# Kernel optimization log

Measured on AMD Instinct MI355X. Metric: run time of the kernel, lower is better.

The kernel has to match this reference:

```python
import jax, jax.numpy as jnp
import numpy as np

D = 512            # model size
H = 8              # num_heads
HD = D // H        # head_size = 64
WIN = 7            # num_keys (payload tokens per window)
QNB = 5            # query_nb for 'mean' aggregation
SCALE = D ** -0.5  # NOTE: torch module scales by size**-0.5, not head_size**-0.5
EPS = 1e-5


def setup_inputs() -> dict:
    key = jax.random.key(0)
    ks = jax.random.split(key, 12)
    B, M = 8, 4096
    w = lambda i: jax.random.normal(ks[i], (D, D), jnp.float32) * 0.02
    return {
        "k": jax.random.normal(ks[0], (B, M, D), jnp.float32),
        "v": jax.random.normal(ks[1], (B, M, D), jnp.float32),
        "q": jax.random.normal(ks[2], (B, M, D), jnp.float32),
        "query_len": 3584,
        "Wk": w(3), "bk": jnp.zeros((D,), jnp.float32),
        "Wv": w(4), "bv": jnp.zeros((D,), jnp.float32),
        "Wq": w(5), "bq": jnp.zeros((D,), jnp.float32),
        "ln_g": jnp.ones((D,), jnp.float32), "ln_b": jnp.zeros((D,), jnp.float32),
        "Wpq": w(6), "bpq": jnp.zeros((D,), jnp.float32),
        "Wpk": w(7), "bpk": jnp.zeros((D,), jnp.float32),
        "Wo": w(8), "bo": jnp.zeros((D,), jnp.float32),
    }


def reference(k, v, q, query_len, Wk, bk, Wv, bv, Wq, bq, ln_g, ln_b, Wpq, bpq, Wpk, bpk, Wo, bo):
    B, M, _ = k.shape
    win_num = -(-query_len // WIN)     # ceil
    per_win = M // win_num

    k = k @ Wk + bk
    v = v @ Wv + bv
    q = q @ Wq + bq

    # 'mean' query aggregation: AvgPool1d(kernel=QNB, stride=1, pad=QNB//2),
    # count_include_pad=True => always divide by QNB (zero-padded)
    qp = jnp.pad(q, ((0, 0), (QNB // 2, QNB // 2), (0, 0)))
    q = sum(qp[:, j:j + M] for j in range(QNB)) / QNB

    # ---- stage 1: DSA (local attention inside each window of per_win tokens)
    resh = lambda x: x.reshape(B, win_num, per_win, H, HD).transpose(0, 1, 3, 2, 4)
    dq, dk, dv = resh(q), resh(k), resh(v)                       # [B,W,H,p,hd]
    attn = jax.nn.softmax(jnp.einsum('bwhqd,bwhkd->bwhqk', dq, dk) * SCALE, axis=-1)
    out = jnp.einsum('bwhqk,bwhkd->bwhqd', attn, dv)
    out = out.transpose(0, 1, 3, 2, 4).reshape(B, win_num, per_win, D)

    win_tok = out[:, :, 0, :]          # [B, W, D] window summary tokens
    attn_x = out[:, :, 1:, :]

    # LayerNorm + exact GELU on window tokens
    mu = win_tok.mean(-1, keepdims=True)
    var = ((win_tok - mu) ** 2).mean(-1, keepdims=True)
    win_tok = (win_tok - mu) / jnp.sqrt(var + EPS) * ln_g + ln_b
    win_tok = jax.nn.gelu(win_tok, approximate=False)

    # ---- stage 2: PSA (attention over window summary tokens)
    pq = (win_tok @ Wpq + bpq).reshape(B, win_num, H, HD).transpose(0, 2, 1, 3)  # [B,H,W,hd]
    pk = (win_tok @ Wpk + bpk).reshape(B, win_num, H, HD).transpose(0, 2, 1, 3)
    pv = attn_x.reshape(B, win_num, WIN, H, HD).transpose(0, 3, 1, 2, 4)
    pv = pv.reshape(B, H, win_num, WIN * HD)

    pattn = jax.nn.softmax(jnp.einsum('bhqd,bhkd->bhqk', pq, pk) * SCALE, axis=-1)
    pout = jnp.einsum('bhqk,bhkd->bhqd', pattn, pv)
    pout = pout.transpose(0, 2, 1, 3).reshape(B, win_num, H, WIN, HD)
    pout = pout.transpose(0, 1, 3, 2, 4).reshape(B, win_num, WIN, D)

    out = (pout + attn_x).reshape(B, win_num * WIN, D)[:, :query_len, :]
    return out @ Wo + bo
```

## Files before the change

kernel.cpp:

```cpp
#include <hip/hip_runtime.h>
#include <hip/hip_bf16.h>
#include <math.h>

#define SCALE_ 0.04419417382415922f
#define EPS_  1e-5f

typedef unsigned short u16;
typedef __attribute__((ext_vector_type(8))) short     bf16x8;
typedef __attribute__((ext_vector_type(4))) float     f32x4;
typedef __attribute__((ext_vector_type(8))) unsigned short u16x8;
typedef __attribute__((ext_vector_type(4))) unsigned short u16x4;

__device__ __forceinline__ u16 f2b(float f) {
  union { float f; unsigned int u; } x; x.f = f;
  unsigned int u = x.u;
  return (u16)((u + 0x7FFFu + ((u >> 16) & 1u)) >> 16);
}
__device__ __forceinline__ float b2f(u16 h) {
  union { unsigned int u; float f; } x; x.u = ((unsigned int)h) << 16;
  return x.f;
}
__device__ __forceinline__ void gload_lds16(const void* g, void* l) {
  __builtin_amdgcn_global_load_lds(
      (const __attribute__((address_space(1))) void*)g,
      (__attribute__((address_space(3))) void*)l, 16, 0, 0);
}

__global__ __launch_bounds__(256) void wconv(
    const float* W0, const float* W1, const float* W2,
    const float* W3, const float* W4, const float* W5, u16* wt)
{
  const float* W;
  switch (blockIdx.z) {
    case 0: W = W0; break; case 1: W = W1; break; case 2: W = W2; break;
    case 3: W = W3; break; case 4: W = W4; break; default: W = W5; break;
  }
  u16* Wt = wt + (size_t)blockIdx.z * 262144;
  const int k0 = blockIdx.x * 64, n0 = blockIdx.y * 64;
  __shared__ float T[64][68];
  const int tid = threadIdx.x;
#pragma unroll
  for (int it = 0; it < 4; ++it) {
    int L = it * 256 + tid;
    int r = L >> 4, cg = L & 15;
    float4 v = *reinterpret_cast<const float4*>(W + (size_t)(k0 + r) * 512 + n0 + cg * 4);
    T[r][cg * 4 + 0] = v.x; T[r][cg * 4 + 1] = v.y;
    T[r][cg * 4 + 2] = v.z; T[r][cg * 4 + 3] = v.w;
  }
  __syncthreads();
#pragma unroll
  for (int it = 0; it < 2; ++it) {
    int L = it * 256 + tid;
    int rn = L >> 3, kg = L & 7;
    u16x8 o;
#pragma unroll
    for (int e = 0; e < 8; ++e) o[e] = f2b(T[kg * 8 + e][rn]);
    *(u16x8*)(Wt + (size_t)(n0 + rn) * 512 + k0 + kg * 8) = o;
  }
}

__global__ __launch_bounds__(512) void gemm_proj(
    const float* A0, const u16* Bt0, const float* bi0, u16* C0,
    const float* A1, const u16* Bt1, const float* bi1, u16* C1,
    const float* A2, const u16* Bt2, const float* bi2, u16* C2)
{
  const float *A, *bias; const u16* Bt; u16* C;
  if (blockIdx.z == 0)      { A = A0; Bt = Bt0; bias = bi0; C = C0; }
  else if (blockIdx.z == 1) { A = A1; Bt = Bt1; bias = bi1; C = C1; }
  else                      { A = A2; Bt = Bt2; bias = bi2; C = C2; }

  __shared__ u16 As[2][4096];
  __shared__ u16 Bs[2][16384];
  const int tid = threadIdx.x;
  const int lane = tid & 63, wid = tid >> 6;
  const int wr = wid >> 2, wcn = wid & 3;
  const int l15 = lane & 15, lh = lane >> 4;
  const int sx = (l15 >> 1) & 3;
  const int m0 = blockIdx.x * 128;

  const int rr = tid >> 2, sp = tid & 3;
  const int ssw = sp ^ ((rr >> 1) & 3);

  const f32x4 fz = {0.f, 0.f, 0.f, 0.f};
  f32x4 acc[4][8];
#pragma unroll
  for (int m = 0; m < 4; ++m)
#pragma unroll
    for (int n = 0; n < 8; ++n) acc[m][n] = fz;

  const int aoff0 = (wr * 64 + l15) * 64 + ((lh ^ sx) << 4);
  const int boff0 = (wcn * 128 + l15) * 64 + ((lh ^ sx) << 4);

  {
#pragma unroll
    for (int it = 0; it < 4; ++it)
      gload_lds16(Bt + (size_t)(it * 128 + rr) * 512 + ssw * 8,
                  (char*)Bs[0] + (it * 512 + wid * 64) * 16);
    const float* ga = A + (size_t)(m0 + rr) * 512 + ssw * 8;
    float4 x0 = *reinterpret_cast<const float4*>(ga);
    float4 x1 = *reinterpret_cast<const float4*>(ga + 4);
    u16x8 o;
    o[0] = f2b(x0.x); o[1] = f2b(x0.y); o[2] = f2b(x0.z); o[3] = f2b(x0.w);
    o[4] = f2b(x1.x); o[5] = f2b(x1.y); o[6] = f2b(x1.z); o[7] = f2b(x1.w);
    *(u16x8*)((char*)As[0] + tid * 16) = o;
  }
  __syncthreads();

#pragma unroll 2
  for (int t = 0; t < 16; ++t) {
    const int cur = t & 1, nxt = cur ^ 1;
    float4 x0 = {0.f,0.f,0.f,0.f}, x1 = {0.f,0.f,0.f,0.f};
    if (t < 15) {
      const int k0 = (t + 1) * 32;
#pragma unroll
      for (int it = 0; it < 4; ++it)
        gload_lds16(Bt + (size_t)(it * 128 + rr) * 512 + k0 + ssw * 8,
                    (char*)Bs[nxt] + (it * 512 + wid * 64) * 16);
      const float* ga = A + (size_t)(m0 + rr) * 512 + k0 + ssw * 8;
      x0 = *reinterpret_cast<const float4*>(ga);
      x1 = *reinterpret_cast<const float4*>(ga + 4);
    }
    bf16x8 af[4], bfr[8];
#pragma unroll
    for (int m = 0; m < 4; ++m)
      af[m] = *(const bf16x8*)((const char*)As[cur] + aoff0 + m * 1024);
#pragma unroll
    for (int n = 0; n < 8; ++n)
      bfr[n] = *(const bf16x8*)((const char*)Bs[cur] + boff0 + n * 1024);
#pragma unroll
    for (int m = 0; m < 4; ++m)
#pragma unroll
      for (int n = 0; n < 8; ++n)
        acc[m][n] = __builtin_amdgcn_mfma_f32_16x16x32_bf16(af[m], bfr[n], acc[m][n], 0, 0, 0);
    if (t < 15) {
      u16x8 o;
      o[0] = f2b(x0.x); o[1] = f2b(x0.y); o[2] = f2b(x0.z); o[3] = f2b(x0.w);
      o[4] = f2b(x1.x); o[5] = f2b(x1.y); o[6] = f2b(x1.z); o[7] = f2b(x1.w);
      *(u16x8*)((char*)As[nxt] + tid * 16) = o;
    }
    __syncthreads();
  }

  const int gn0 = wcn * 128 + l15;
  float bv[8];
#pragma unroll
  for (int n = 0; n < 8; ++n) bv[n] = bias[gn0 + n * 16];
#pragma unroll
  for (int m = 0; m < 4; ++m)
#pragma unroll
    for (int reg = 0; reg < 4; ++reg) {
      int gm = m0 + wr * 64 + m * 16 + lh * 4 + reg;
#pragma unroll
      for (int n = 0; n < 8; ++n)
        C[(size_t)gm * 512 + gn0 + n * 16] = f2b(acc[m][n][reg] + bv[n]);
    }
}

__global__ __launch_bounds__(512) void gemm_out(
    const u16* __restrict__ A, const u16* __restrict__ Bt,
    const float* __restrict__ bias, float* __restrict__ C)
{
  __shared__ u16 As[2][4096];
  __shared__ u16 Bs[2][16384];
  const int tid = threadIdx.x;
  const int lane = tid & 63, wid = tid >> 6;
  const int wr = wid >> 2, wcn = wid & 3;
  const int l15 = lane & 15, lh = lane >> 4;
  const int sx = (l15 >> 1) & 3;
  const int m0 = blockIdx.x * 128;
  const int rr = tid >> 2, sp = tid & 3;
  const int ssw = sp ^ ((rr >> 1) & 3);

  const f32x4 fz = {0.f, 0.f, 0.f, 0.f};
  f32x4 acc[4][8];
#pragma unroll
  for (int m = 0; m < 4; ++m)
#pragma unroll
    for (int n = 0; n < 8; ++n) acc[m][n] = fz;

  const int aoff0 = (wr * 64 + l15) * 64 + ((lh ^ sx) << 4);
  const int boff0 = (wcn * 128 + l15) * 64 + ((lh ^ sx) << 4);

  {
#pragma unroll
    for (int it = 0; it < 4; ++it)
      gload_lds16(Bt + (size_t)(it * 128 + rr) * 512 + ssw * 8,
                  (char*)Bs[0] + (it * 512 + wid * 64) * 16);
    gload_lds16(A + (size_t)(m0 + rr) * 512 + ssw * 8,
                (char*)As[0] + (wid * 64) * 16);
  }
  __syncthreads();

#pragma unroll 2
  for (int t = 0; t < 16; ++t) {
    const int cur = t & 1, nxt = cur ^ 1;
    if (t < 15) {
      const int k0 = (t + 1) * 32;
#pragma unroll
      for (int it = 0; it < 4; ++it)
        gload_lds16(Bt + (size_t)(it * 128 + rr) * 512 + k0 + ssw * 8,
                    (char*)Bs[nxt] + (it * 512 + wid * 64) * 16);
      gload_lds16(A + (size_t)(m0 + rr) * 512 + k0 + ssw * 8,
                  (char*)As[nxt] + (wid * 64) * 16);
    }
    bf16x8 af[4], bfr[8];
#pragma unroll
    for (int m = 0; m < 4; ++m)
      af[m] = *(const bf16x8*)((const char*)As[cur] + aoff0 + m * 1024);
#pragma unroll
    for (int n = 0; n < 8; ++n)
      bfr[n] = *(const bf16x8*)((const char*)Bs[cur] + boff0 + n * 1024);
#pragma unroll
    for (int m = 0; m < 4; ++m)
#pragma unroll
      for (int n = 0; n < 8; ++n)
        acc[m][n] = __builtin_amdgcn_mfma_f32_16x16x32_bf16(af[m], bfr[n], acc[m][n], 0, 0, 0);
    __syncthreads();
  }

  const int gn0 = wcn * 128 + l15;
  float bv[8];
#pragma unroll
  for (int n = 0; n < 8; ++n) bv[n] = bias[gn0 + n * 16];
#pragma unroll
  for (int m = 0; m < 4; ++m)
#pragma unroll
    for (int reg = 0; reg < 4; ++reg) {
      int gm = m0 + wr * 64 + m * 16 + lh * 4 + reg;
#pragma unroll
      for (int n = 0; n < 8; ++n)
        C[(size_t)gm * 512 + gn0 + n * 16] = acc[m][n][reg] + bv[n];
    }
}

__global__ __launch_bounds__(256) void gemm_pp(
    const u16* __restrict__ A,
    const u16* __restrict__ Bt0, const float* __restrict__ bi0, u16* __restrict__ C0,
    const u16* __restrict__ Bt1, const float* __restrict__ bi1, u16* __restrict__ C1)
{
  const u16* Bt; const float* bias; u16* C;
  if (blockIdx.z == 0) { Bt = Bt0; bias = bi0; C = C0; }
  else                 { Bt = Bt1; bias = bi1; C = C1; }

  __shared__ u16 As[8192];
  __shared__ u16 Bs[8192];
  const int tid = threadIdx.x;
  const int lane = tid & 63, wid = tid >> 6;
  const int wr = wid >> 1, wc = wid & 1;
  const int l15 = lane & 15, lh = lane >> 4, l7 = lane & 7;
  const int m0 = blockIdx.x * 128, n0 = blockIdx.y * 128;

  const f32x4 fz = {0.f, 0.f, 0.f, 0.f};
  f32x4 acc[4][4];
#pragma unroll
  for (int m = 0; m < 4; ++m)
#pragma unroll
    for (int n = 0; n < 4; ++n) acc[m][n] = fz;

  int aoff[2], boff[2];
#pragma unroll
  for (int kh = 0; kh < 2; ++kh) {
    int slot = ((kh * 4 + lh) ^ l7) << 4;
    aoff[kh] = (wr * 64 + l15) * 128 + slot;
    boff[kh] = (wc * 64 + l15) * 128 + slot;
  }

  for (int k0 = 0; k0 < 512; k0 += 64) {
    __syncthreads();
#pragma unroll
    for (int it = 0; it < 4; ++it) {
      int L = it * 256 + tid;
      int r = L >> 3, s = L & 7;
      int c = s ^ (r & 7);
      gload_lds16(A  + (size_t)(m0 + r) * 512 + k0 + c * 8,
                  (char*)As + (it * 256 + wid * 64) * 16);
      gload_lds16(Bt + (size_t)(n0 + r) * 512 + k0 + c * 8,
                  (char*)Bs + (it * 256 + wid * 64) * 16);
    }
    __syncthreads();
#pragma unroll
    for (int kh = 0; kh < 2; ++kh) {
      bf16x8 af[4], bfr[4];
#pragma unroll
      for (int m = 0; m < 4; ++m)
        af[m] = *(const bf16x8*)((const char*)As + aoff[kh] + m * 2048);
#pragma unroll
      for (int n = 0; n < 4; ++n)
        bfr[n] = *(const bf16x8*)((const char*)Bs + boff[kh] + n * 2048);
#pragma unroll
      for (int m = 0; m < 4; ++m)
#pragma unroll
        for (int n = 0; n < 4; ++n)
          acc[m][n] = __builtin_amdgcn_mfma_f32_16x16x32_bf16(af[m], bfr[n], acc[m][n], 0, 0, 0);
    }
  }

  const int gn0 = n0 + wc * 64 + l15;
  float bv[4];
#pragma unroll
  for (int n = 0; n < 4; ++n) bv[n] = bias[gn0 + n * 16];
#pragma unroll
  for (int m = 0; m < 4; ++m)
#pragma unroll
    for (int reg = 0; reg < 4; ++reg) {
      int gm = m0 + wr * 64 + m * 16 + lh * 4 + reg;
#pragma unroll
      for (int n = 0; n < 4; ++n)
        C[(size_t)gm * 512 + gn0 + n * 16] = f2b(acc[m][n][reg] + bv[n]);
    }
}

__global__ __launch_bounds__(256) void qk_mfma(
    const u16* __restrict__ pq, const u16* __restrict__ pk, u16* __restrict__ expS)
{
  __shared__ u16 As[8192];
  __shared__ u16 Bs[8192];
  const int tid = threadIdx.x;
  const int lane = tid & 63, wid = tid >> 6;
  const int wr = wid >> 1, wc = wid & 1;
  const int l15 = lane & 15, lh = lane >> 4, l7 = lane & 7;
  const int bh = blockIdx.z, b = bh >> 3, h = bh & 7;
  const int wq0 = blockIdx.x * 128, wk0 = blockIdx.y * 128;

  const f32x4 fz = {0.f, 0.f, 0.f, 0.f};
  f32x4 acc[4][4];
#pragma unroll
  for (int m = 0; m < 4; ++m)
#pragma unroll
    for (int n = 0; n < 4; ++n) acc[m][n] = fz;

#pragma unroll
  for (int it = 0; it < 4; ++it) {
    int L = it * 256 + tid;
    int r = L >> 3, s = L & 7;
    int c = s ^ (r & 7);
    gload_lds16(pq + ((size_t)b * 512 + wq0 + r) * 512 + h * 64 + c * 8,
                (char*)As + (it * 256 + wid * 64) * 16);
    gload_lds16(pk + ((size_t)b * 512 + wk0 + r) * 512 + h * 64 + c * 8,
                (char*)Bs + (it * 256 + wid * 64) * 16);
  }
  __syncthreads();

#pragma unroll
  for (int kh = 0; kh < 2; ++kh) {
    int slot = ((kh * 4 + lh) ^ l7) << 4;
    int aoff = (wr * 64 + l15) * 128 + slot;
    int boff = (wc * 64 + l15) * 128 + slot;
    bf16x8 af[4], bfr[4];
#pragma unroll
    for (int m = 0; m < 4; ++m)
      af[m] = *(const bf16x8*)((const char*)As + aoff + m * 2048);
#pragma unroll
    for (int n = 0; n < 4; ++n)
      bfr[n] = *(const bf16x8*)((const char*)Bs + boff + n * 2048);
#pragma unroll
    for (int m = 0; m < 4; ++m)
#pragma unroll
      for (int n = 0; n < 4; ++n)
        acc[m][n] = __builtin_amdgcn_mfma_f32_16x16x32_bf16(af[m], bfr[n], acc[m][n], 0, 0, 0);
  }

  const int gn0 = wk0 + wc * 64 + l15;
#pragma unroll
  for (int m = 0; m < 4; ++m)
#pragma unroll
    for (int reg = 0; reg < 4; ++reg) {
      int gm = wq0 + wr * 64 + m * 16 + lh * 4 + reg;
#pragma unroll
      for (int n = 0; n < 4; ++n)
        expS[((size_t)bh * 512 + gm) * 512 + gn0 + n * 16] =
            f2b(expf(acc[m][n][reg] * SCALE_));
    }
}

__global__ __launch_bounds__(64) void attn_win(
    const u16* kp, const u16* vp, const u16* qp0, u16* attn)
{
  const int h = blockIdx.x, w = blockIdx.y, b = blockIdx.z;
  const int t = threadIdx.x;
  __shared__ float ks[8][68], vs[8][68], qr[12][68], qs[8][68], Ps[8][9];
  const size_t base = ((size_t)b * 4096 + (size_t)w * 8) * 512 + h * 64;

  {
    int i = t >> 3, dg = t & 7;
    u16x8 kv = *(const u16x8*)(kp + base + (size_t)i * 512 + dg * 8);
    u16x8 vv = *(const u16x8*)(vp + base + (size_t)i * 512 + dg * 8);
#pragma unroll
    for (int e = 0; e < 8; ++e) {
      ks[i][dg * 8 + e] = b2f(kv[e]);
      vs[i][dg * 8 + e] = b2f(vv[e]);
    }
  }
#pragma unroll
  for (int l = 0; l < 2; ++l) {
    int L = t + l * 64;
    if (L < 96) {
      int i = L >> 3, dg = L & 7;
      int m = w * 8 - 2 + i;
      if (m >= 0 && m < 4096) {
        u16x8 qv = *(const u16x8*)(qp0 + ((size_t)b * 4096 + m) * 512 + h * 64 + dg * 8);
#pragma unroll
        for (int e = 0; e < 8; ++e) qr[i][dg * 8 + e] = b2f(qv[e]);
      } else {
#pragma unroll
        for (int e = 0; e < 8; ++e) qr[i][dg * 8 + e] = 0.0f;
      }
    }
  }
  __syncthreads();
#pragma unroll
  for (int j = 0; j < 8; ++j)
    qs[j][t] = 0.2f * (qr[j][t] + qr[j + 1][t] + qr[j + 2][t] + qr[j + 3][t] + qr[j + 4][t]);
  __syncthreads();

  const int qi = t >> 3, kj = t & 7;
  float s = 0.0f;
#pragma unroll
  for (int d = 0; d < 64; ++d) s = fmaf(qs[qi][d], ks[kj][d], s);
  s *= SCALE_;
  float mx = s;
  mx = fmaxf(mx, __shfl_xor(mx, 1));
  mx = fmaxf(mx, __shfl_xor(mx, 2));
  mx = fmaxf(mx, __shfl_xor(mx, 4));
  float e = expf(s - mx);
  float sum = e;
  sum += __shfl_xor(sum, 1);
  sum += __shfl_xor(sum, 2);
  sum += __shfl_xor(sum, 4);
  Ps[qi][kj] = e / sum;
  __syncthreads();

  float o[8];
#pragma unroll
  for (int c = 0; c < 8; ++c) o[c] = 0.0f;
#pragma unroll
  for (int tt = 0; tt < 8; ++tt) {
    float pw = Ps[qi][tt];
#pragma unroll
    for (int c = 0; c < 8; ++c) o[c] = fmaf(pw, vs[tt][kj * 8 + c], o[c]);
  }
  u16x8 ov;
#pragma unroll
  for (int c = 0; c < 8; ++c) ov[c] = f2b(o[c]);
  *(u16x8*)(attn + base + (size_t)qi * 512 + kj * 8) = ov;
}

__global__ __launch_bounds__(256) void pvt_build(const u16* attn, u16* pvT)
{
  const int bh = blockIdx.x;
  const int b = bh >> 3, h = bh & 7;
  const int w0 = blockIdx.y * 32;
  __shared__ u16 TL[448 * 40];
  const int tid = threadIdx.x;
#pragma unroll
  for (int it = 0; it < 8; ++it) {
    int L = it * 256 + tid;
    int dg = L & 7, r = L >> 3;
    int w2l = r >> 3, tt = r & 7;
    if (tt < 7) {
      int m = 8 * (w0 + w2l) + tt + 1;
      u16x8 v = *(const u16x8*)(attn + ((size_t)b * 4096 + m) * 512 + h * 64 + dg * 8);
#pragma unroll
      for (int e = 0; e < 8; ++e)
        TL[(tt * 64 + dg * 8 + e) * 40 + w2l] = v[e];
    }
  }
  __syncthreads();
#pragma unroll
  for (int it = 0; it < 7; ++it) {
    int L = it * 256 + tid;
    int n = L >> 2, seg = L & 3;
    u16x8 v = *(const u16x8*)(&TL[n * 40 + seg * 8]);
    *(u16x8*)(pvT + ((size_t)bh * 448 + n) * 512 + w0 + seg * 8) = v;
  }
}

__global__ __launch_bounds__(64) void ln_gelu(
    const u16* attn, const float* g, const float* be, u16* wt)
{
  const int r = blockIdx.x;
  const int b = r >> 9, w = r & 511;
  const int t = threadIdx.x;
  const u16* x = attn + (((size_t)b * 4096) + (size_t)w * 8) * 512;

  u16x8 v = *(const u16x8*)(x + t * 8);
  float xv[8];
  float s1 = 0.f, s2 = 0.f;
#pragma unroll
  for (int e = 0; e < 8; ++e) {
    xv[e] = b2f(v[e]);
    s1 += xv[e]; s2 += xv[e] * xv[e];
  }
#pragma unroll
  for (int off = 1; off < 64; off <<= 1) {
    s1 += __shfl_xor(s1, off);
    s2 += __shfl_xor(s2, off);
  }
  const float mu  = s1 * (1.0f / 512.0f);
  const float var = s2 * (1.0f / 512.0f) - mu * mu;
  const float inv = 1.0f / sqrtf(var + EPS_);

  const int d0 = t * 8;
  float4 g0 = *reinterpret_cast<const float4*>(g + d0);
  float4 g1 = *reinterpret_cast<const float4*>(g + d0 + 4);
  float4 b0 = *reinterpret_cast<const float4*>(be + d0);
  float4 b1 = *reinterpret_cast<const float4*>(be + d0 + 4);
  float gv[8] = {g0.x, g0.y, g0.z, g0.w, g1.x, g1.y, g1.z, g1.w};
  float bvv[8] = {b0.x, b0.y, b0.z, b0.w, b1.x, b1.y, b1.z, b1.w};
  const float k2 = 0.70710678118654752f;
  u16x8 ov;
#pragma unroll
  for (int e = 0; e < 8; ++e) {
    float y = (xv[e] - mu) * inv * gv[e] + bvv[e];
    ov[e] = f2b(0.5f * y * (1.0f + erff(y * k2)));
  }
  *(u16x8*)(wt + (size_t)r * 512 + d0) = ov;
}

__global__ __launch_bounds__(256) void rs_inv(const u16* expS, float* rsinv)
{
  const int row = blockIdx.x * 4 + (threadIdx.x >> 6);
  const int t = threadIdx.x & 63;
  u16x8 v = *(const u16x8*)(expS + (size_t)row * 512 + t * 8);
  float s = 0.f;
#pragma unroll
  for (int e = 0; e < 8; ++e) s += b2f(v[e]);
#pragma unroll
  for (int off = 1; off < 64; off <<= 1) s += __shfl_xor(s, off);
  if (t == 0) rsinv[row] = 1.0f / s;
}

__global__ __launch_bounds__(256) void pv_mfma(
    const u16* __restrict__ expS, const u16* __restrict__ pvT,
    const float* __restrict__ rsinv, const u16* __restrict__ attn,
    u16* __restrict__ X2)
{
  __shared__ u16 As[8192];
  __shared__ u16 Bs[4096];
  const int tid = threadIdx.x;
  const int lane = tid & 63, wid = tid >> 6;
  const int wr = wid >> 1, wc = wid & 1;
  const int l15 = lane & 15, lh = lane >> 4, l7 = lane & 7;
  const int bh = blockIdx.z, b = bh >> 3, h = bh & 7;
  const int m0 = blockIdx.x * 128;
  const int nt = blockIdx.y;

  const f32x4 fz = {0.f, 0.f, 0.f, 0.f};
  f32x4 acc[4][2];
#pragma unroll
  for (int m = 0; m < 4; ++m)
#pragma unroll
    for (int n = 0; n < 2; ++n) acc[m][n] = fz;

  int aoff[2], boff[2];
#pragma unroll
  for (int kh = 0; kh < 2; ++kh) {
    int slot = ((kh * 4 + lh) ^ l7) << 4;
    aoff[kh] = (wr * 64 + l15) * 128 + slot;
    boff[kh] = (wc * 32 + l15) * 128 + slot;
  }

  for (int k0 = 0; k0 < 512; k0 += 64) {
    __syncthreads();
#pragma unroll
    for (int it = 0; it < 4; ++it) {
      int L = it * 256 + tid;
      int r = L >> 3, s = L & 7;
      int c = s ^ (r & 7);
      gload_lds16(expS + ((size_t)bh * 512 + m0 + r) * 512 + k0 + c * 8,
                  (char*)As + (it * 256 + wid * 64) * 16);
    }
#pragma unroll
    for (int it = 0; it < 2; ++it) {
      int L = it * 256 + tid;
      int r = L >> 3, s = L & 7;
      int c = s ^ (r & 7);
      gload_lds16(pvT + ((size_t)bh * 448 + nt * 64 + r) * 512 + k0 + c * 8,
                  (char*)Bs + (it * 256 + wid * 64) * 16);
    }
    __syncthreads();
#pragma unroll
    for (int kh = 0; kh < 2; ++kh) {
      bf16x8 af[4], bfr[2];
#pragma unroll
      for (int m = 0; m < 4; ++m)
        af[m] = *(const bf16x8*)((const char*)As + aoff[kh] + m * 2048);
#pragma unroll
      for (int n = 0; n < 2; ++n)
        bfr[n] = *(const bf16x8*)((const char*)Bs + boff[kh] + n * 2048);
#pragma unroll
      for (int m = 0; m < 4; ++m)
#pragma unroll
        for (int n = 0; n < 2; ++n)
          acc[m][n] = __builtin_amdgcn_mfma_f32_16x16x32_bf16(af[m], bfr[n], acc[m][n], 0, 0, 0);
    }
  }

#pragma unroll
  for (int m = 0; m < 4; ++m)
#pragma unroll
    for (int reg = 0; reg < 4; ++reg) {
      int gm = m0 + wr * 64 + m * 16 + lh * 4 + reg;
      float ri = rsinv[bh * 512 + gm];
#pragma unroll
      for (int n = 0; n < 2; ++n) {
        int d = wc * 32 + n * 16 + l15;
        float res = b2f(attn[((size_t)b * 4096 + gm * 8 + nt + 1) * 512 + h * 64 + d]);
        X2[((size_t)b * 3584 + gm * 7 + nt) * 512 + h * 64 + d] =
            f2b(acc[m][n][reg] * ri + res);
      }
    }
}

extern "C" void kernel_launch(void* const* d_in, const int* in_sizes, int n_in,
                              void* d_out, int out_size, void* d_ws, size_t ws_size,
                              hipStream_t stream)
{
  const float* k_in = (const float*)d_in[0];
  const float* v_in = (const float*)d_in[1];
  const float* q_in = (const float*)d_in[2];
  const float* Wk  = (const float*)d_in[4];
  const float* bk  = (const float*)d_in[5];
  const float* Wv  = (const float*)d_in[6];
  const float* bv  = (const float*)d_in[7];
  const float* Wq  = (const float*)d_in[8];
  const float* bq  = (const float*)d_in[9];
  const float* lng = (const float*)d_in[10];
  const float* lnb = (const float*)d_in[11];
  const float* Wpq = (const float*)d_in[12];
  const float* bpq = (const float*)d_in[13];
  const float* Wpk = (const float*)d_in[14];
  const float* bpk = (const float*)d_in[15];
  const float* Wo  = (const float*)d_in[16];
  const float* bo  = (const float*)d_in[17];
  float* out = (float*)d_out;

  char* ws = (char*)d_ws;
  const size_t MB = 1024 * 1024;
  u16* wtb  = (u16*)(ws);
  u16* kp   = (u16*)(ws + 16 * MB);
  u16* vp   = (u16*)(ws + 52 * MB);
  u16* qp0  = (u16*)(ws + 88 * MB);
  u16* attn = (u16*)(ws + 124 * MB);
  u16*   wt    = (u16*)(ws + 16 * MB);
  u16*   pq    = (u16*)(ws + 20 * MB);
  u16*   pk    = (u16*)(ws + 28 * MB);
  float* rsinv = (float*)(ws + 36 * MB);
  u16*   expS  = (u16*)(ws + 40 * MB);
  u16*   pvT   = (u16*)(ws + 76 * MB);
  u16*   X2    = (u16*)(ws + 160 * MB);

  u16* Wkt  = wtb;
  u16* Wvt  = wtb + 1 * 262144;
  u16* Wqt  = wtb + 2 * 262144;
  u16* Wpqt = wtb + 3 * 262144;
  u16* Wpkt = wtb + 4 * 262144;
  u16* Wot  = wtb + 5 * 262144;

  wconv<<<dim3(8, 8, 6), 256, 0, stream>>>(Wk, Wv, Wq, Wpq, Wpk, Wo, wtb);

  gemm_proj<<<dim3(256, 1, 3), 512, 0, stream>>>(
      k_in, Wkt, bk, kp,
      v_in, Wvt, bv, vp,
      q_in, Wqt, bq, qp0);

  attn_win<<<dim3(8, 512, 8), 64, 0, stream>>>(kp, vp, qp0, attn);
  pvt_build<<<dim3(64, 16), 256, 0, stream>>>(attn, pvT);
  ln_gelu<<<4096, 64, 0, stream>>>(attn, lng, lnb, wt);

  gemm_pp<<<dim3(32, 4, 2), 256, 0, stream>>>(
      wt, Wpqt, bpq, pq, Wpkt, bpk, pk);

  qk_mfma<<<dim3(4, 4, 64), 256, 0, stream>>>(pq, pk, expS);
  rs_inv<<<8192, 256, 0, stream>>>(expS, rsinv);
  pv_mfma<<<dim3(4, 7, 64), 256, 0, stream>>>(expS, pvT, rsinv, attn, X2);

  gemm_out<<<dim3(224, 1, 1), 512, 0, stream>>>(X2, Wot, bo, out);
}
```

Baseline: 281.1 us.

## Retile projection GEMM to 128x128 blocks with direct global B fragment loads

The QKV projection GEMM changes from a 512-thread block covering 128 rows by the full 512 columns to a 256-thread block covering 128x128 tiles, launched over four column tiles. B fragments are now read straight from global memory into registers rather than staged in LDS, and the A tile uses a 64-wide k-step with XOR swizzling. This cuts LDS use and raises occupancy, at the cost of reading and converting the fp32 A rows four times and issuing uncached-in-LDS B loads. Separately, the pv_mfma grid swaps its x and y dimensions so neighbouring blocks share the same row tile.

```diff
diff --git a/kernel.cpp b/kernel.cpp
--- a/kernel.cpp
+++ b/kernel.cpp
@@ -59,7 +59,7 @@
   }
 }
 
-__global__ __launch_bounds__(512) void gemm_proj(
+__global__ __launch_bounds__(256, 3) void gemm_proj(
     const float* A0, const u16* Bt0, const float* bi0, u16* C0,
     const float* A1, const u16* Bt1, const float* bi1, u16* C1,
     const float* A2, const u16* Bt2, const float* bi2, u16* C2)
@@ -69,89 +69,110 @@
   else if (blockIdx.z == 1) { A = A1; Bt = Bt1; bias = bi1; C = C1; }
   else                      { A = A2; Bt = Bt2; bias = bi2; C = C2; }
 
-  __shared__ u16 As[2][4096];
-  __shared__ u16 Bs[2][16384];
+  __shared__ u16 As[2][8192];
   const int tid = threadIdx.x;
   const int lane = tid & 63, wid = tid >> 6;
-  const int wr = wid >> 2, wcn = wid & 3;
-  const int l15 = lane & 15, lh = lane >> 4;
-  const int sx = (l15 >> 1) & 3;
-  const int m0 = blockIdx.x * 128;
-
-  const int rr = tid >> 2, sp = tid & 3;
-  const int ssw = sp ^ ((rr >> 1) & 3);
+  const int wr = wid >> 1, wc = wid & 1;
+  const int l15 = lane & 15, lh = lane >> 4, l7 = lane & 7;
+  const int m0 = blockIdx.x * 128, n0 = blockIdx.y * 128;
 
   const f32x4 fz = {0.f, 0.f, 0.f, 0.f};
-  f32x4 acc[4][8];
-#pragma unroll
-  for (int m = 0; m < 4; ++m)
-#pragma unroll
-    for (int n = 0; n < 8; ++n) acc[m][n] = fz;
-
-  const int aoff0 = (wr * 64 + l15) * 64 + ((lh ^ sx) << 4);
-  const int boff0 = (wcn * 128 + l15) * 64 + ((lh ^ sx) << 4);
-
-  {
-#pragma unroll
-    for (int it = 0; it < 4; ++it)
-      gload_lds16(Bt + (size_t)(it * 128 + rr) * 512 + ssw * 8,
-                  (char*)Bs[0] + (it * 512 + wid * 64) * 16);
-    const float* ga = A + (size_t)(m0 + rr) * 512 + ssw * 8;
-    float4 x0 = *reinterpret_cast<const float4*>(ga);
-    float4 x1 = *reinterpret_cast<const float4*>(ga + 4);
+  f32x4 acc[4][4];
+#pragma unroll
+  for (int m = 0; m < 4; ++m)
+#pragma unroll
+    for (int n = 0; n < 4; ++n) acc[m][n] = fz;
+
+  int aoff[2];
+#pragma unroll
+  for (int kh = 0; kh < 2; ++kh)
+    aoff[kh] = (wr * 64 + l15) * 128 + (((kh * 4 + lh) ^ l7) << 4);
+
+  const u16* Brow[4];
+#pragma unroll
+  for (int nf = 0; nf < 4; ++nf)
+    Brow[nf] = Bt + (size_t)(n0 + wc * 64 + nf * 16 + l15) * 512 + lh * 8;
+
+  float4 xa[4], xb[4];
+#pragma unroll
+  for (int it = 0; it < 4; ++it) {
+    int L = it * 256 + tid;
+    int r = L >> 3, s = L & 7;
+    int c = s ^ (r & 7);
+    const float* ga = A + (size_t)(m0 + r) * 512 + c * 8;
+    xa[it] = *reinterpret_cast<const float4*>(ga);
+    xb[it] = *reinterpret_cast<const float4*>(ga + 4);
+  }
+#pragma unroll
+  for (int it = 0; it < 4; ++it) {
+    int L = it * 256 + tid;
     u16x8 o;
-    o[0] = f2b(x0.x); o[1] = f2b(x0.y); o[2] = f2b(x0.z); o[3] = f2b(x0.w);
-    o[4] = f2b(x1.x); o[5] = f2b(x1.y); o[6] = f2b(x1.z); o[7] = f2b(x1.w);
-    *(u16x8*)((char*)As[0] + tid * 16) = o;
+    o[0] = f2b(xa[it].x); o[1] = f2b(xa[it].y);
+    o[2] = f2b(xa[it].z); o[3] = f2b(xa[it].w);
+    o[4] = f2b(xb[it].x); o[5] = f2b(xb[it].y);
+    o[6] = f2b(xb[it].z); o[7] = f2b(xb[it].w);
+    *(u16x8*)((char*)As[0] + L * 16) = o;
   }
   __syncthreads();
 
-#pragma unroll 2
-  for (int t = 0; t < 16; ++t) {
-    const int cur = t & 1, nxt = cur ^ 1;
-    float4 x0 = {0.f,0.f,0.f,0.f}, x1 = {0.f,0.f,0.f,0.f};
-    if (t < 15) {
-      const int k0 = (t + 1) * 32;
-#pragma unroll
-      for (int it = 0; it < 4; ++it)
-        gload_lds16(Bt + (size_t)(it * 128 + rr) * 512 + k0 + ssw * 8,
-                    (char*)Bs[nxt] + (it * 512 + wid * 64) * 16);
-      const float* ga = A + (size_t)(m0 + rr) * 512 + k0 + ssw * 8;
-      x0 = *reinterpret_cast<const float4*>(ga);
-      x1 = *reinterpret_cast<const float4*>(ga + 4);
-    }
-    bf16x8 af[4], bfr[8];
-#pragma unroll
-    for (int m = 0; m < 4; ++m)
-      af[m] = *(const bf16x8*)((const char*)As[cur] + aoff0 + m * 1024);
-#pragma unroll
-    for (int n = 0; n < 8; ++n)
-      bfr[n] = *(const bf16x8*)((const char*)Bs[cur] + boff0 + n * 1024);
-#pragma unroll
-    for (int m = 0; m < 4; ++m)
-#pragma unroll
-      for (int n = 0; n < 8; ++n)
-        acc[m][n] = __builtin_amdgcn_mfma_f32_16x16x32_bf16(af[m], bfr[n], acc[m][n], 0, 0, 0);
-    if (t < 15) {
-      u16x8 o;
-      o[0] = f2b(x0.x); o[1] = f2b(x0.y); o[2] = f2b(x0.z); o[3] = f2b(x0.w);
-      o[4] = f2b(x1.x); o[5] = f2b(x1.y); o[6] = f2b(x1.z); o[7] = f2b(x1.w);
-      *(u16x8*)((char*)As[nxt] + tid * 16) = o;
+  for (int t = 0; t < 8; ++t) {
+    const int cur = t & 1;
+    if (t < 7) {
+      const int kn = (t + 1) * 64;
+#pragma unroll
+      for (int it = 0; it < 4; ++it) {
+        int L = it * 256 + tid;
+        int r = L >> 3, s = L & 7;
+        int c = s ^ (r & 7);
+        const float* ga = A + (size_t)(m0 + r) * 512 + kn + c * 8;
+        xa[it] = *reinterpret_cast<const float4*>(ga);
+        xb[it] = *reinterpret_cast<const float4*>(ga + 4);
+      }
+    }
+    bf16x8 bfr[2][4];
+#pragma unroll
+    for (int kh = 0; kh < 2; ++kh)
+#pragma unroll
+      for (int nf = 0; nf < 4; ++nf)
+        bfr[kh][nf] = *(const bf16x8*)(Brow[nf] + t * 64 + kh * 32);
+#pragma unroll
+    for (int kh = 0; kh < 2; ++kh) {
+      bf16x8 af[4];
+#pragma unroll
+      for (int m = 0; m < 4; ++m)
+        af[m] = *(const bf16x8*)((const char*)As[cur] + aoff[kh] + m * 2048);
+#pragma unroll
+      for (int m = 0; m < 4; ++m)
+#pragma unroll
+        for (int n = 0; n < 4; ++n)
+          acc[m][n] = __builtin_amdgcn_mfma_f32_16x16x32_bf16(af[m], bfr[kh][n], acc[m][n], 0, 0, 0);
+    }
+    if (t < 7) {
+#pragma unroll
+      for (int it = 0; it < 4; ++it) {
+        int L = it * 256 + tid;
+        u16x8 o;
+        o[0] = f2b(xa[it].x); o[1] = f2b(xa[it].y);
+        o[2] = f2b(xa[it].z); o[3] = f2b(xa[it].w);
+        o[4] = f2b(xb[it].x); o[5] = f2b(xb[it].y);
+        o[6] = f2b(xb[it].z); o[7] = f2b(xb[it].w);
+        *(u16x8*)((char*)As[cur ^ 1] + L * 16) = o;
+      }
     }
     __syncthreads();
   }
 
-  const int gn0 = wcn * 128 + l15;
-  float bv[8];
-#pragma unroll
-  for (int n = 0; n < 8; ++n) bv[n] = bias[gn0 + n * 16];
+  const int gn0 = n0 + wc * 64 + l15;
+  float bv[4];
+#pragma unroll
+  for (int n = 0; n < 4; ++n) bv[n] = bias[gn0 + n * 16];
 #pragma unroll
   for (int m = 0; m < 4; ++m)
 #pragma unroll
     for (int reg = 0; reg < 4; ++reg) {
       int gm = m0 + wr * 64 + m * 16 + lh * 4 + reg;
 #pragma unroll
-      for (int n = 0; n < 8; ++n)
+      for (int n = 0; n < 4; ++n)
         C[(size_t)gm * 512 + gn0 + n * 16] = f2b(acc[m][n][reg] + bv[n]);
     }
 }
@@ -542,8 +563,8 @@
   const int wr = wid >> 1, wc = wid & 1;
   const int l15 = lane & 15, lh = lane >> 4, l7 = lane & 7;
   const int bh = blockIdx.z, b = bh >> 3, h = bh & 7;
-  const int m0 = blockIdx.x * 128;
-  const int nt = blockIdx.y;
+  const int m0 = blockIdx.y * 128;
+  const int nt = blockIdx.x;
 
   const f32x4 fz = {0.f, 0.f, 0.f, 0.f};
   f32x4 acc[4][2];
@@ -659,7 +680,7 @@
 
   wconv<<<dim3(8, 8, 6), 256, 0, stream>>>(Wk, Wv, Wq, Wpq, Wpk, Wo, wtb);
 
-  gemm_proj<<<dim3(256, 1, 3), 512, 0, stream>>>(
+  gemm_proj<<<dim3(256, 4, 3), 256, 0, stream>>>(
       k_in, Wkt, bk, kp,
       v_in, Wvt, bv, vp,
       q_in, Wqt, bq, qp0);
@@ -673,7 +694,7 @@
 
   qk_mfma<<<dim3(4, 4, 64), 256, 0, stream>>>(pq, pk, expS);
   rs_inv<<<8192, 256, 0, stream>>>(expS, rsinv);
-  pv_mfma<<<dim3(4, 7, 64), 256, 0, stream>>>(expS, pvT, rsinv, attn, X2);
+  pv_mfma<<<dim3(7, 4, 64), 256, 0, stream>>>(expS, pvT, rsinv, attn, X2);
 
   gemm_out<<<dim3(224, 1, 1), 512, 0, stream>>>(X2, Wot, bo, out);
 }
```

Result: slower. 383.3 us (+36.3%).
